# Optimization experiments

Hardware: AMD Instinct MI355X
Metric: run time of the kernel (lower is better)

Reference implementation:

```python
import jax, jax.numpy as jnp
import numpy as np

H = 16      # num_heads
D = 64      # head_dim
BQ = 64     # block_size_q
BKV = 64    # block_size_kv


def setup_inputs() -> dict:
    key = jax.random.key(0)
    ks = jax.random.split(key, 5)
    B, S, dim = 2, 2048, 1024
    x = jax.random.normal(ks[0], (B, S, dim), dtype=jnp.float32)
    Wq = jax.random.normal(ks[1], (dim, H * D), dtype=jnp.float32) * 0.02
    Wk = jax.random.normal(ks[2], (dim, H * D), dtype=jnp.float32) * 0.02
    Wv = jax.random.normal(ks[3], (dim, H * D), dtype=jnp.float32) * 0.02
    Wo = jax.random.normal(ks[4], (H * D, dim), dtype=jnp.float32) * 0.02
    return {"x": x, "Wq": Wq, "Wk": Wk, "Wv": Wv, "Wo": Wo}


def _flash_tiled(q, k, v, scale):
    # q,k,v: (B, H, S, D). Non-causal tiled attention with online softmax,
    # faithfully replicating the source's per-iteration division by l_new.
    B, nh, S, d = q.shape
    nq, nkv = S // BQ, S // BKV
    qb = q.reshape(B, nh, nq, BQ, d)                       # all q blocks at once (outer loop vectorized)
    kb = k.reshape(B, nh, nkv, BKV, d).transpose(2, 0, 1, 3, 4)  # (nkv, B, H, BKV, D)
    vb = v.reshape(B, nh, nkv, BKV, d).transpose(2, 0, 1, 3, 4)

    o0 = jnp.zeros((B, nh, nq, BQ, d), q.dtype)
    m0 = jnp.full((B, nh, nq, BQ), -jnp.inf, q.dtype)
    l0 = jnp.zeros((B, nh, nq, BQ), q.dtype)

    def step(carry, kv):
        o, m, l = carry
        kj, vj = kv
        s = jnp.einsum('bhnqd,bhkd->bhnqk', qb, kj) * scale   # (B,H,nq,BQ,BKV)
        m_new = jnp.maximum(m, s.max(axis=-1))
        p = jnp.exp(s - m_new[..., None])
        alpha = jnp.exp(m - m_new)
        l_new = alpha * l + p.sum(axis=-1)
        # NOTE: division by l_new every iteration, as in the source module.
        o_new = (alpha[..., None] * o + jnp.einsum('bhnqk,bhkd->bhnqd', p, vj)) / l_new[..., None]
        return (o_new, m_new, l_new), None

    (o, _, _), _ = jax.lax.scan(step, (o0, m0, l0), (kb, vb))
    return o.reshape(B, nh, S, d)


def reference(x, Wq, Wk, Wv, Wo):
    B, S, dim = x.shape
    scale = D ** -0.5
    q = (x @ Wq).reshape(B, S, H, D).transpose(0, 2, 1, 3)
    k = (x @ Wk).reshape(B, S, H, D).transpose(0, 2, 1, 3)
    v = (x @ Wv).reshape(B, S, H, D).transpose(0, 2, 1, 3)
    o = _flash_tiled(q, k, v, scale)                       # (B,H,S,D)
    out = o.transpose(0, 2, 1, 3).reshape(B, S, H * D)
    return out @ Wo
```

## Files before the change

kernel.cpp:

```cpp
#include <hip/hip_runtime.h>
#include <hip/hip_bf16.h>
#include <math.h>

#define BB   2
#define SS   2048
#define DIM  1024
#define NH   16
#define HD   64
#define MTOT (BB * SS)

typedef unsigned short ushortT;
typedef __attribute__((ext_vector_type(8))) short short8v;
typedef __attribute__((ext_vector_type(4))) float float4v;
typedef __attribute__((ext_vector_type(16))) float float16v;

union FragU { short8v v; unsigned short us[8]; unsigned int u[4]; };

__device__ inline unsigned short f2bf(float x) {
    unsigned u = __builtin_bit_cast(unsigned, x);
    u += 0x7fffu + ((u >> 16) & 1u);
    return (unsigned short)(u >> 16);
}
__device__ inline float bf2f(unsigned short h) {
    unsigned u = ((unsigned)h) << 16;
    return __builtin_bit_cast(float, u);
}
__device__ inline void split_tr(float x, unsigned short& hi, unsigned short& lo) {
    unsigned u = __builtin_bit_cast(unsigned, x);
    hi = (unsigned short)(u >> 16);
    float hf = __builtin_bit_cast(float, u & 0xffff0000u);
    lo = (unsigned short)(__builtin_bit_cast(unsigned, x - hf) >> 16);
}
__device__ inline void split4(const float4& x, short4& hi, short4& lo) {
    unsigned short h0 = f2bf(x.x), h1 = f2bf(x.y), h2 = f2bf(x.z), h3 = f2bf(x.w);
    hi = make_short4((short)h0, (short)h1, (short)h2, (short)h3);
    lo = make_short4((short)f2bf(x.x - bf2f(h0)), (short)f2bf(x.y - bf2f(h1)),
                     (short)f2bf(x.z - bf2f(h2)), (short)f2bf(x.w - bf2f(h3)));
}
__device__ inline void gld_lds16(const void* g, void* l) {
    __builtin_amdgcn_global_load_lds(
        (const __attribute__((address_space(1))) void*)g,
        (__attribute__((address_space(3))) void*)l, 16, 0, 0);
}
__device__ inline unsigned cvt_pk_bf16(float a, float b) {
    unsigned r;
    asm("v_cvt_pk_bf16_f32 %0, %1, %2" : "=v"(r) : "v"(a), "v"(b));
    return r;
}
__device__ inline void permlane32_swap(unsigned &a, unsigned &b) {
    asm("v_permlane32_swap_b32 %0, %1" : "+v"(a), "+v"(b));
}

__global__ __launch_bounds__(256) void convert_split_kernel(
    const float* __restrict__ in, ushortT* __restrict__ hi, ushortT* __restrict__ lo, int n4)
{
    int t = blockIdx.x * 256 + threadIdx.x;
    if (t < n4) {
        float4 x = ((const float4*)in)[t];
        short4 h, l; split4(x, h, l);
        ((short4*)hi)[t] = h;
        ((short4*)lo)[t] = l;
    }
}

__global__ __launch_bounds__(256) void transpose_split_kernel(
    const float* __restrict__ W0, const float* __restrict__ W1,
    const float* __restrict__ W2, const float* __restrict__ W3,
    ushortT* __restrict__ WtH, ushortT* __restrict__ WtL)
{
    const int z = blockIdx.z;
    const float* __restrict__ W = (z == 0) ? W0 : (z == 1) ? W1 : (z == 2) ? W2 : W3;
    ushortT* H = WtH + (size_t)z * 1024 * 1024;
    ushortT* L = WtL + (size_t)z * 1024 * 1024;

    __shared__ float T[64][65];
    const int k0 = blockIdx.y * 64, n0 = blockIdx.x * 64;
    const int tid = threadIdx.x;
    const int c4 = (tid & 15) * 4;

#pragma unroll
    for (int i = 0; i < 4; i++) {
        int r = (tid >> 4) + 16 * i;
        *(float4*)&T[r][c4] = *(const float4*)(W + (size_t)(k0 + r) * 1024 + n0 + c4);
    }
    __syncthreads();
#pragma unroll
    for (int i = 0; i < 4; i++) {
        int n = (tid >> 4) + 16 * i;
        float4 vv = make_float4(T[c4 + 0][n], T[c4 + 1][n], T[c4 + 2][n], T[c4 + 3][n]);
        short4 h, l; split4(vv, h, l);
        *(short4*)&H[(size_t)(n0 + n) * 1024 + k0 + c4] = h;
        *(short4*)&L[(size_t)(n0 + n) * 1024 + k0 + c4] = l;
    }
}

__global__ __launch_bounds__(256) void kv_convert_kernel(
    const float* __restrict__ kw,
    ushortT* __restrict__ KhG, ushortT* __restrict__ KlG)
{
    const int jb = blockIdx.x, bh = blockIdx.y;
    const int b = bh >> 4, h = bh & 15;

    __shared__ float T[64][68];
    const int tid = threadIdx.x;
    const size_t ibase = (size_t)b * SS * DIM + (size_t)h * HD + (size_t)(jb * 64) * DIM;
    const int c4 = (tid & 15) * 4;
#pragma unroll
    for (int i = 0; i < 4; i++) {
        int r = (tid >> 4) + 16 * i;
        *(float4*)&T[r][c4] = *(const float4*)(kw + ibase + (size_t)r * DIM + c4);
    }
    __syncthreads();

    ushortT* oh = KhG + (size_t)(bh * 32 + jb) * 4096;
    ushortT* ol = KlG + (size_t)(bh * 32 + jb) * 4096;

#pragma unroll
    for (int i = 0; i < 2; i++) {
        const int s = tid + i * 256;
        const int f = s >> 6;
        const int lane = s & 63;
        const int ds = f >> 1, kvt = f & 1;
        const int kv = kvt * 32 + (lane & 31);
        const int d0 = ds * 16 + (lane >> 5) * 8;
        ushortT hv[8], lv[8];
#pragma unroll
        for (int j = 0; j < 8; j++) split_tr(T[kv][d0 + j], hv[j], lv[j]);
        *(short4*)&oh[s * 8]     = *(short4*)&hv[0];
        *(short4*)&oh[s * 8 + 4] = *(short4*)&hv[4];
        *(short4*)&ol[s * 8]     = *(short4*)&lv[0];
        *(short4*)&ol[s * 8 + 4] = *(short4*)&lv[4];
    }
}

__global__ __launch_bounds__(256, 2) void gemm_bt_split_kernel(
    const ushortT* __restrict__ Ah, const ushortT* __restrict__ Al,
    const ushortT* __restrict__ BtH, const ushortT* __restrict__ BtL,
    float* __restrict__ Y0, float* __restrict__ Y1,
    ushortT* __restrict__ VhG, ushortT* __restrict__ VlG)
{
    const int z = blockIdx.z;
    const ushortT* __restrict__ Bh = BtH + (size_t)z * 1024 * 1024;
    const ushortT* __restrict__ Bl = BtL + (size_t)z * 1024 * 1024;

    const int K = 1024, N = 1024;
    const int wid  = blockIdx.x + (blockIdx.y << 3);
    const int work = ((wid & 7) << 5) + (wid >> 3);
    const int m0 = (work >> 3) * 128;
    const int n0 = (work & 7) * 128;

    __shared__ __align__(16) ushortT AhS[128 * 64];
    __shared__ __align__(16) ushortT AlS[128 * 64];
    __shared__ __align__(16) ushortT BhS[128 * 64];
    __shared__ __align__(16) ushortT BlS[128 * 64];

    const int tid  = threadIdx.x;
    const int wave = tid >> 6, lane = tid & 63;
    const int quad = lane >> 4, l15 = lane & 15;
    const int wm = wave >> 1, wn = wave & 1;
    const int rx = l15 & 7;

    float4v acc[4][4];
#pragma unroll
    for (int i = 0; i < 4; i++)
#pragma unroll
        for (int j = 0; j < 4; j++) acc[i][j] = (float4v){0.f, 0.f, 0.f, 0.f};

    for (int k0 = 0; k0 < K; k0 += 64) {
        __syncthreads();
#pragma unroll
        for (int i = 0; i < 4; i++) {
            const int s = tid + i * 256;
            const int r = s >> 3;
            const int kk = ((s & 7) ^ (r & 7)) * 8;
            gld_lds16(Ah + (size_t)(m0 + r) * K + k0 + kk, &AhS[s * 8]);
            gld_lds16(Al + (size_t)(m0 + r) * K + k0 + kk, &AlS[s * 8]);
            gld_lds16(Bh + (size_t)(n0 + r) * K + k0 + kk, &BhS[s * 8]);
            gld_lds16(Bl + (size_t)(n0 + r) * K + k0 + kk, &BlS[s * 8]);
        }
        __syncthreads();

#pragma unroll
        for (int ks = 0; ks < 2; ks++) {
            FragU ah[4], al[4], bh[4], bl[4];
#pragma unroll
            for (int t = 0; t < 4; t++) {
                const int ra = wm * 64 + t * 16 + l15;
                const int rb = wn * 64 + t * 16 + l15;
                const int boff = ((ks * 4 + quad) ^ rx) * 8;
                ah[t].v = *(const short8v*)&AhS[ra * 64 + boff];
                al[t].v = *(const short8v*)&AlS[ra * 64 + boff];
                bh[t].v = *(const short8v*)&BhS[rb * 64 + boff];
                bl[t].v = *(const short8v*)&BlS[rb * 64 + boff];
            }
#pragma unroll
            for (int mt = 0; mt < 4; mt++)
#pragma unroll
                for (int nt = 0; nt < 4; nt++) {
                    acc[mt][nt] = __builtin_amdgcn_mfma_f32_16x16x32_bf16(ah[mt].v, bh[nt].v, acc[mt][nt], 0, 0, 0);
                    acc[mt][nt] = __builtin_amdgcn_mfma_f32_16x16x32_bf16(ah[mt].v, bl[nt].v, acc[mt][nt], 0, 0, 0);
                    acc[mt][nt] = __builtin_amdgcn_mfma_f32_16x16x32_bf16(al[mt].v, bh[nt].v, acc[mt][nt], 0, 0, 0);
                }
        }
    }

    if (z == 2) {
        const int b  = m0 >> 11;
        const int jb = ((m0 & 2047) >> 6) + wm;
        const int h  = (n0 >> 6) + wn;
        const size_t tb = (size_t)((b * 16 + h) * 32 + jb) * 4096;
        ushortT* vh = VhG + tb;
        ushortT* vl = VlG + tb;
#pragma unroll
        for (int mt = 0; mt < 4; mt++)
#pragma unroll
            for (int nt = 0; nt < 4; nt++) {
                const int off = ((((nt >> 1) * 4 + mt) * 64 +
                                  (quad >> 1) * 32 + (nt & 1) * 16 + l15) * 8) +
                                (quad & 1) * 4;
                float4 vv = make_float4(acc[mt][nt][0], acc[mt][nt][1],
                                        acc[mt][nt][2], acc[mt][nt][3]);
                unsigned short h0, l0, h1, l1, h2, l2, h3, l3;
                split_tr(vv.x, h0, l0); split_tr(vv.y, h1, l1);
                split_tr(vv.z, h2, l2); split_tr(vv.w, h3, l3);
                *(short4*)&vh[off] = make_short4((short)h0, (short)h1, (short)h2, (short)h3);
                *(short4*)&vl[off] = make_short4((short)l0, (short)l1, (short)l2, (short)l3);
            }
    } else {
        float* __restrict__ Y = (z == 0) ? Y0 : Y1;
#pragma unroll
        for (int mt = 0; mt < 4; mt++)
#pragma unroll
            for (int r = 0; r < 4; r++) {
                const int row = m0 + wm * 64 + mt * 16 + quad * 4 + r;
                float* yp = Y + (size_t)row * N + n0 + wn * 64 + l15;
#pragma unroll
                for (int nt = 0; nt < 4; nt++)
                    yp[nt * 16] = acc[mt][nt][r];
            }
    }
}

__global__ __launch_bounds__(256, 2) void gemm_bt64_kernel(
    const ushortT* __restrict__ Ah, const ushortT* __restrict__ Al,
    const ushortT* __restrict__ Bh, const ushortT* __restrict__ Bl,
    float* __restrict__ Y)
{
    const int K = 1024, N = 1024;
    const int wid  = blockIdx.x + (blockIdx.y << 3);
    const int work = ((wid & 7) << 6) + (wid >> 3);
    const int m0 = (work >> 3) * 64;
    const int n0 = (work & 7) * 128;

    __shared__ __align__(16) ushortT AhS[64 * 64];
    __shared__ __align__(16) ushortT AlS[64 * 64];
    __shared__ __align__(16) ushortT BhS[128 * 64];
    __shared__ __align__(16) ushortT BlS[128 * 64];

    const int tid  = threadIdx.x;
    const int wave = tid >> 6, lane = tid & 63;
    const int quad = lane >> 4, l15 = lane & 15;
    const int rx = l15 & 7;

    float4v acc[4][2];
#pragma unroll
    for (int i = 0; i < 4; i++)
#pragma unroll
        for (int j = 0; j < 2; j++) acc[i][j] = (float4v){0.f, 0.f, 0.f, 0.f};

    for (int k0 = 0; k0 < K; k0 += 64) {
        __syncthreads();
#pragma unroll
        for (int i = 0; i < 2; i++) {
            const int s = tid + i * 256;
            const int r = s >> 3;
            const int kk = ((s & 7) ^ (r & 7)) * 8;
            gld_lds16(Ah + (size_t)(m0 + r) * K + k0 + kk, &AhS[s * 8]);
            gld_lds16(Al + (size_t)(m0 + r) * K + k0 + kk, &AlS[s * 8]);
        }
#pragma unroll
        for (int i = 0; i < 4; i++) {
            const int s = tid + i * 256;
            const int r = s >> 3;
            const int kk = ((s & 7) ^ (r & 7)) * 8;
            gld_lds16(Bh + (size_t)(n0 + r) * K + k0 + kk, &BhS[s * 8]);
            gld_lds16(Bl + (size_t)(n0 + r) * K + k0 + kk, &BlS[s * 8]);
        }
        __syncthreads();

#pragma unroll
        for (int ks = 0; ks < 2; ks++) {
            FragU ah[4], al[4], bh[2], bl[2];
#pragma unroll
            for (int t = 0; t < 4; t++) {
                const int ra = t * 16 + l15;
                const int boff = ((ks * 4 + quad) ^ rx) * 8;
                ah[t].v = *(const short8v*)&AhS[ra * 64 + boff];
                al[t].v = *(const short8v*)&AlS[ra * 64 + boff];
            }
#pragma unroll
            for (int t = 0; t < 2; t++) {
                const int rb = wave * 32 + t * 16 + l15;
                const int boff = ((ks * 4 + quad) ^ rx) * 8;
                bh[t].v = *(const short8v*)&BhS[rb * 64 + boff];
                bl[t].v = *(const short8v*)&BlS[rb * 64 + boff];
            }
#pragma unroll
            for (int mt = 0; mt < 4; mt++)
#pragma unroll
                for (int nt = 0; nt < 2; nt++) {
                    acc[mt][nt] = __builtin_amdgcn_mfma_f32_16x16x32_bf16(ah[mt].v, bh[nt].v, acc[mt][nt], 0, 0, 0);
                    acc[mt][nt] = __builtin_amdgcn_mfma_f32_16x16x32_bf16(ah[mt].v, bl[nt].v, acc[mt][nt], 0, 0, 0);
                    acc[mt][nt] = __builtin_amdgcn_mfma_f32_16x16x32_bf16(al[mt].v, bh[nt].v, acc[mt][nt], 0, 0, 0);
                }
        }
    }

#pragma unroll
    for (int mt = 0; mt < 4; mt++)
#pragma unroll
        for (int r = 0; r < 4; r++) {
            const int row = m0 + mt * 16 + quad * 4 + r;
            float* yp = Y + (size_t)row * N + n0 + wave * 32 + l15;
#pragma unroll
            for (int nt = 0; nt < 2; nt++)
                yp[nt * 16] = acc[mt][nt][r];
        }
}

__global__ __launch_bounds__(256, 2) void attn_mfma_kernel(
    const float* __restrict__ q,
    const ushortT* __restrict__ KhG, const ushortT* __restrict__ KlG,
    const ushortT* __restrict__ VhG, const ushortT* __restrict__ VlG,
    ushortT* __restrict__ Oh, ushortT* __restrict__ Ol)
{
    __shared__ __align__(16) ushortT SMEM[32768];

    const int tid  = threadIdx.x;
    const int wave = tid >> 6, lane = tid & 63;
    const int l31 = lane & 31, hi5 = lane >> 5;
    const int wid  = blockIdx.x + (blockIdx.y << 4);
    const int work = ((wid & 7) << 6) + (wid >> 3);
    const int qx = work & 15;
    const int bh = work >> 4;
    const int b = bh >> 4, h = bh & 15;
    const size_t base = (size_t)b * SS * DIM + (size_t)h * HD;
    const int qs0 = qx * 128 + wave * 32;
    const int lane8 = lane * 8;
    const int sl0 = wave * 128 + lane, sl1 = sl0 + 64;

    ushortT* K0 = SMEM;
    ushortT* K1 = SMEM + 8192;
    ushortT* V0 = SMEM + 16384;
    ushortT* V1 = SMEM + 24576;

    const float qscale = 0.125f * 1.4426950408889634f;
    FragU Qh[4], Ql[4];
    {
        const int qrow = qs0 + l31;
#pragma unroll
        for (int ds = 0; ds < 4; ds++) {
            const float* p0 = q + base + (size_t)qrow * DIM + ds * 16 + hi5 * 8;
            float4 a = *(const float4*)(p0);
            float4 c = *(const float4*)(p0 + 4);
            float e[8] = {a.x, a.y, a.z, a.w, c.x, c.y, c.z, c.w};
#pragma unroll
            for (int j = 0; j < 8; j++) {
                float x = e[j] * qscale;
                unsigned short hs = f2bf(x);
                Qh[ds].us[j] = hs;
                Ql[ds].us[j] = f2bf(x - bf2f(hs));
            }
        }
    }

    float16v Oacc[2];
#pragma unroll
    for (int dt = 0; dt < 2; dt++)
        Oacc[dt] = (float16v){0.f,0.f,0.f,0.f,0.f,0.f,0.f,0.f,
                              0.f,0.f,0.f,0.f,0.f,0.f,0.f,0.f};

    float m_run = -INFINITY;
    float l_run = 0.f;
    float inv_prev = 1.0f;

    auto stage_K = [&](int t, ushortT* dst) {
        const size_t tb = (size_t)(bh * 32 + t) * 4096;
        gld_lds16(KhG + tb + sl0 * 8, &dst[sl0 * 8]);
        gld_lds16(KhG + tb + sl1 * 8, &dst[sl1 * 8]);
        gld_lds16(KlG + tb + sl0 * 8, &dst[4096 + sl0 * 8]);
        gld_lds16(KlG + tb + sl1 * 8, &dst[4096 + sl1 * 8]);
    };
    auto stage_V = [&](int t, ushortT* dst) {
        const size_t tb = (size_t)(bh * 32 + t) * 4096;
        gld_lds16(VhG + tb + sl0 * 8, &dst[sl0 * 8]);
        gld_lds16(VhG + tb + sl1 * 8, &dst[sl1 * 8]);
        gld_lds16(VlG + tb + sl0 * 8, &dst[4096 + sl0 * 8]);
        gld_lds16(VlG + tb + sl1 * 8, &dst[4096 + sl1 * 8]);
    };

    auto qk = [&](const ushortT* Kb, float16v (&st)[2]) {
        const ushortT* KhS = Kb;
        const ushortT* KlS = Kb + 4096;
#pragma unroll
        for (int t = 0; t < 2; t++)
            st[t] = (float16v){0.f,0.f,0.f,0.f,0.f,0.f,0.f,0.f,
                               0.f,0.f,0.f,0.f,0.f,0.f,0.f,0.f};
#pragma unroll
        for (int ds = 0; ds < 4; ds++) {
            FragU kh0, kl0, kh1, kl1;
            kh0.v = *(const short8v*)&KhS[(ds * 2 + 0) * 512 + lane8];
            kl0.v = *(const short8v*)&KlS[(ds * 2 + 0) * 512 + lane8];
            kh1.v = *(const short8v*)&KhS[(ds * 2 + 1) * 512 + lane8];
            kl1.v = *(const short8v*)&KlS[(ds * 2 + 1) * 512 + lane8];
            st[0] = __builtin_amdgcn_mfma_f32_32x32x16_bf16(kh0.v, Qh[ds].v, st[0], 0, 0, 0);
            st[0] = __builtin_amdgcn_mfma_f32_32x32x16_bf16(kh0.v, Ql[ds].v, st[0], 0, 0, 0);
            st[0] = __builtin_amdgcn_mfma_f32_32x32x16_bf16(kl0.v, Qh[ds].v, st[0], 0, 0, 0);
            st[1] = __builtin_amdgcn_mfma_f32_32x32x16_bf16(kh1.v, Qh[ds].v, st[1], 0, 0, 0);
            st[1] = __builtin_amdgcn_mfma_f32_32x32x16_bf16(kh1.v, Ql[ds].v, st[1], 0, 0, 0);
            st[1] = __builtin_amdgcn_mfma_f32_32x32x16_bf16(kl1.v, Qh[ds].v, st[1], 0, 0, 0);
        }
    };

    auto finish = [&](float16v (&st)[2], const ushortT* Vb) {
        const ushortT* VhS = Vb;
        const ushortT* VlS = Vb + 4096;
        float wscale;
        {
            float g[8];
#pragma unroll
            for (int t = 0; t < 2; t++)
#pragma unroll
                for (int i = 0; i < 4; i++)
                    g[t * 4 + i] = fmaxf(fmaxf(st[t][4 * i], st[t][4 * i + 1]),
                                         fmaxf(st[t][4 * i + 2], st[t][4 * i + 3]));
            float vmax = fmaxf(fmaxf(fmaxf(g[0], g[1]), fmaxf(g[2], g[3])),
                               fmaxf(fmaxf(g[4], g[5]), fmaxf(g[6], g[7])));
            vmax = fmaxf(vmax, __shfl_xor(vmax, 32, 64));
            const float mn = fmaxf(m_run, vmax);
            const float al = __builtin_amdgcn_exp2f(m_run - mn);

            float ssum = 0.f;
#pragma unroll
            for (int t = 0; t < 2; t++)
#pragma unroll
                for (int r = 0; r < 16; r++) {
                    const float p = __builtin_amdgcn_exp2f(st[t][r] - mn);
                    st[t][r] = p;
                    ssum += p;
                }
            ssum += __shfl_xor(ssum, 32, 64);
            const float ln = al * l_run + ssum;
            wscale = al * inv_prev;
            inv_prev = __builtin_amdgcn_rcpf(ln);
            m_run = mn;
            l_run = ln;
        }

#pragma unroll
        for (int dt = 0; dt < 2; dt++)
#pragma unroll
            for (int r = 0; r < 16; r++)
                Oacc[dt][r] *= wscale;

#pragma unroll
        for (int kvs = 0; kvs < 4; kvs++) {
            const int kvt = kvs >> 1;
            const int R = (kvs & 1) * 8;
            float p0 = st[kvt][R + 0], p1 = st[kvt][R + 1];
            float p2 = st[kvt][R + 2], p3 = st[kvt][R + 3];
            float p4 = st[kvt][R + 4], p5 = st[kvt][R + 5];
            float p6 = st[kvt][R + 6], p7 = st[kvt][R + 7];
            unsigned X0 = cvt_pk_bf16(p0, p1), X1 = cvt_pk_bf16(p2, p3);
            unsigned Y0 = cvt_pk_bf16(p4, p5), Y1 = cvt_pk_bf16(p6, p7);
            float e0 = p0 - __builtin_bit_cast(float, X0 << 16);
            float e1 = p1 - __builtin_bit_cast(float, X0 & 0xffff0000u);
            float e2 = p2 - __builtin_bit_cast(float, X1 << 16);
            float e3 = p3 - __builtin_bit_cast(float, X1 & 0xffff0000u);
            float e4 = p4 - __builtin_bit_cast(float, Y0 << 16);
            float e5 = p5 - __builtin_bit_cast(float, Y0 & 0xffff0000u);
            float e6 = p6 - __builtin_bit_cast(float, Y1 << 16);
            float e7 = p7 - __builtin_bit_cast(float, Y1 & 0xffff0000u);
            unsigned Z0 = cvt_pk_bf16(e0, e1), Z1 = cvt_pk_bf16(e2, e3);
            unsigned W0 = cvt_pk_bf16(e4, e5), W1 = cvt_pk_bf16(e6, e7);
            permlane32_swap(X0, Y0);
            permlane32_swap(X1, Y1);
            permlane32_swap(Z0, W0);
            permlane32_swap(Z1, W1);
            FragU Phf, Plf;
            Phf.u[0] = X0; Phf.u[1] = X1; Phf.u[2] = Y0; Phf.u[3] = Y1;
            Plf.u[0] = Z0; Plf.u[1] = Z1; Plf.u[2] = W0; Plf.u[3] = W1;

#pragma unroll
            for (int dt = 0; dt < 2; dt++) {
                FragU vh, vl;
                vh.v = *(const short8v*)&VhS[(dt * 4 + kvs) * 512 + lane8];
                vl.v = *(const short8v*)&VlS[(dt * 4 + kvs) * 512 + lane8];
                Oacc[dt] = __builtin_amdgcn_mfma_f32_32x32x16_bf16(vh.v, Phf.v, Oacc[dt], 0, 0, 0);
                Oacc[dt] = __builtin_amdgcn_mfma_f32_32x32x16_bf16(vl.v, Phf.v, Oacc[dt], 0, 0, 0);
                Oacc[dt] = __builtin_amdgcn_mfma_f32_32x32x16_bf16(vh.v, Plf.v, Oacc[dt], 0, 0, 0);
            }
        }
    };

    float16v stA[2], stB[2];

    stage_K(0, K0);
    stage_K(1, K1);
    stage_V(0, V0);
    __syncthreads();
    qk(K0, stA);
    __syncthreads();

    auto iter = [&](int jb, float16v (&SC)[2], float16v (&SN)[2],
                    ushortT* Kc, ushortT* Kn, ushortT* Vc, ushortT* Vn) {
        if (jb <= 29) stage_K(jb + 2, Kc);
        if (jb <= 30) stage_V(jb + 1, Vn);
        if (jb <= 30) qk(Kn, SN);
        finish(SC, Vc);
        __syncthreads();
    };

    for (int jb = 0; jb < 32; jb += 2) {
        iter(jb,     stA, stB, K0, K1, V0, V1);
        iter(jb + 1, stB, stA, K1, K0, V1, V0);
    }

#pragma unroll
    for (int dt = 0; dt < 2; dt++)
#pragma unroll
        for (int r = 0; r < 16; r++)
            Oacc[dt][r] *= inv_prev;

    float* EP = ((float*)SMEM) + wave * 1056;
    const int qq = lane >> 1, dh = (lane & 1) * 16;
#pragma unroll
    for (int dt = 0; dt < 2; dt++) {
#pragma unroll
        for (int g = 0; g < 4; g++) {
            float4 wv = make_float4(Oacc[dt][4 * g + 0], Oacc[dt][4 * g + 1],
                                    Oacc[dt][4 * g + 2], Oacc[dt][4 * g + 3]);
            *(float4*)&EP[l31 * 33 + g * 8 + hi5 * 4] = wv;
        }
        float vals[16];
#pragma unroll
        for (int k4 = 0; k4 < 4; k4++)
            *(float4*)&vals[k4 * 4] = *(const float4*)&EP[qq * 33 + dh + k4 * 4];

        unsigned ho[8], lo8[8];
#pragma unroll
        for (int kk = 0; kk < 8; kk++) {
            unsigned short h0, l0, h1, l1;
            split_tr(vals[2 * kk], h0, l0);
            split_tr(vals[2 * kk + 1], h1, l1);
            ho[kk]  = (unsigned)h0 | ((unsigned)h1 << 16);
            lo8[kk] = (unsigned)l0 | ((unsigned)l1 << 16);
        }
        const int qrow = qs0 + qq;
        const size_t off = (size_t)(b * SS + qrow) * DIM + h * HD + dt * 32 + dh;
        *(uint4*)&Oh[off]     = make_uint4(ho[0], ho[1], ho[2], ho[3]);
        *(uint4*)&Oh[off + 8] = make_uint4(ho[4], ho[5], ho[6], ho[7]);
        *(uint4*)&Ol[off]     = make_uint4(lo8[0], lo8[1], lo8[2], lo8[3]);
        *(uint4*)&Ol[off + 8] = make_uint4(lo8[4], lo8[5], lo8[6], lo8[7]);
    }
}

extern "C" void kernel_launch(void* const* d_in, const int* in_sizes, int n_in,
                              void* d_out, int out_size, void* d_ws, size_t ws_size,
                              hipStream_t stream)
{
    const float* x  = (const float*)d_in[0];
    const float* Wq = (const float*)d_in[1];
    const float* Wk = (const float*)d_in[2];
    const float* Wv = (const float*)d_in[3];
    const float* Wo = (const float*)d_in[4];
    float* out = (float*)d_out;

    char* w = (char*)d_ws;
    float*   qw  = (float*)(w);
    float*   kw  = (float*)(w + ((size_t)16 << 20));
    ushortT* VhG = (ushortT*)(w + ((size_t)32 << 20));
    ushortT* VlG = (ushortT*)(w + ((size_t)40 << 20));
    ushortT* XhS = (ushortT*)(w + ((size_t)48 << 20));
    ushortT* XlS = (ushortT*)(w + ((size_t)56 << 20));
    ushortT* WtH = (ushortT*)(w + ((size_t)64 << 20));
    ushortT* WtL = (ushortT*)(w + ((size_t)72 << 20));
    ushortT* KhG = (ushortT*)(w + ((size_t)80 << 20));
    ushortT* KlG = (ushortT*)(w + ((size_t)88 << 20));
    ushortT* OhS = (ushortT*)kw;
    ushortT* OlS = (ushortT*)(w + ((size_t)24 << 20));

    dim3 blk(256);
    const int n4 = MTOT * DIM / 4;

    convert_split_kernel<<<dim3(n4 / 256), blk, 0, stream>>>(x, XhS, XlS, n4);
    transpose_split_kernel<<<dim3(16, 16, 4), blk, 0, stream>>>(Wq, Wk, Wv, Wo, WtH, WtL);

    gemm_bt_split_kernel<<<dim3(8, 32, 3), blk, 0, stream>>>(
        XhS, XlS, WtH, WtL, qw, kw, VhG, VlG);

    kv_convert_kernel<<<dim3(32, 32), blk, 0, stream>>>(kw, KhG, KlG);

    attn_mfma_kernel<<<dim3(16, 32), blk, 0, stream>>>(qw, KhG, KlG, VhG, VlG, OhS, OlS);

    gemm_bt64_kernel<<<dim3(8, 64), blk, 0, stream>>>(
        OhS, OlS, WtH + (size_t)3 * 1024 * 1024, WtL + (size_t)3 * 1024 * 1024,
        out);
}
```

Baseline: 284.3 us.

## Double-buffer LDS in split-bf16 GEMM kernels with 32-wide K stages

Both projection GEMM kernels now use two LDS buffers with a K-step of 32 instead of one buffer with a K-step of 64. The next stage's global-to-LDS loads are issued before computing on the current buffer, removing the load-then-barrier-then-compute serialization. The XOR swizzle is adapted to 4-chunk rows. Halving the K-step doubles the number of barriers, and the asynchronous LDS loads rely on the barrier to make data visible, so overlap depends on how the compiler places vmcnt waits.

Result: slower. 306.3 us (+7.7%).

```diff
diff --git a/kernel.cpp b/kernel.cpp
--- a/kernel.cpp
+++ b/kernel.cpp
@@ -149,16 +149,13 @@
     const int m0 = (work >> 3) * 128;
     const int n0 = (work & 7) * 128;
 
-    __shared__ __align__(16) ushortT AhS[128 * 64];
-    __shared__ __align__(16) ushortT AlS[128 * 64];
-    __shared__ __align__(16) ushortT BhS[128 * 64];
-    __shared__ __align__(16) ushortT BlS[128 * 64];
+    __shared__ __align__(16) ushortT SMEM[32768];
 
     const int tid  = threadIdx.x;
     const int wave = tid >> 6, lane = tid & 63;
     const int quad = lane >> 4, l15 = lane & 15;
     const int wm = wave >> 1, wn = wave & 1;
-    const int rx = l15 & 7;
+    const int rk = (l15 ^ (l15 >> 2)) & 3;
 
     float4v acc[4][4];
 #pragma unroll
@@ -166,42 +163,54 @@
 #pragma unroll
         for (int j = 0; j < 4; j++) acc[i][j] = (float4v){0.f, 0.f, 0.f, 0.f};
 
-    for (int k0 = 0; k0 < K; k0 += 64) {
+    auto stage = [&](int t, int bsel) {
+        ushortT* S = SMEM + bsel * 16384;
+        const int k0 = t * 32;
+#pragma unroll
+        for (int i = 0; i < 2; i++) {
+            const int s = tid + i * 256;
+            const int r = s >> 2;
+            const int kk = (((s & 3) ^ (r ^ (r >> 2))) & 3) * 8;
+            gld_lds16(Ah + (size_t)(m0 + r) * K + k0 + kk, &S[s * 8]);
+            gld_lds16(Al + (size_t)(m0 + r) * K + k0 + kk, &S[4096 + s * 8]);
+            gld_lds16(Bh + (size_t)(n0 + r) * K + k0 + kk, &S[8192 + s * 8]);
+            gld_lds16(Bl + (size_t)(n0 + r) * K + k0 + kk, &S[12288 + s * 8]);
+        }
+    };
+
+    auto compute = [&](int bsel) {
+        const ushortT* S = SMEM + bsel * 16384;
+        FragU ah[4], al[4], bh[4], bl[4];
+        const int boff = (quad ^ rk) * 8;
+#pragma unroll
+        for (int t = 0; t < 4; t++) {
+            const int ra = wm * 64 + t * 16 + l15;
+            const int rb = wn * 64 + t * 16 + l15;
+            ah[t].v = *(const short8v*)&S[ra * 32 + boff];
+            al[t].v = *(const short8v*)&S[4096 + ra * 32 + boff];
+            bh[t].v = *(const short8v*)&S[8192 + rb * 32 + boff];
+            bl[t].v = *(const short8v*)&S[12288 + rb * 32 + boff];
+        }
+#pragma unroll
+        for (int mt = 0; mt < 4; mt++)
+#pragma unroll
+            for (int nt = 0; nt < 4; nt++) {
+                acc[mt][nt] = __builtin_amdgcn_mfma_f32_16x16x32_bf16(ah[mt].v, bh[nt].v, acc[mt][nt], 0, 0, 0);
+                acc[mt][nt] = __builtin_amdgcn_mfma_f32_16x16x32_bf16(ah[mt].v, bl[nt].v, acc[mt][nt], 0, 0, 0);
+                acc[mt][nt] = __builtin_amdgcn_mfma_f32_16x16x32_bf16(al[mt].v, bh[nt].v, acc[mt][nt], 0, 0, 0);
+            }
+    };
+
+    stage(0, 0);
+    __syncthreads();
+
+    for (int t = 0; t < 32; t += 2) {
+        if (t < 31) stage(t + 1, 1);
+        compute(0);
         __syncthreads();
-#pragma unroll
-        for (int i = 0; i < 4; i++) {
-            const int s = tid + i * 256;
-            const int r = s >> 3;
-            const int kk = ((s & 7) ^ (r & 7)) * 8;
-            gld_lds16(Ah + (size_t)(m0 + r) * K + k0 + kk, &AhS[s * 8]);
-            gld_lds16(Al + (size_t)(m0 + r) * K + k0 + kk, &AlS[s * 8]);
-            gld_lds16(Bh + (size_t)(n0 + r) * K + k0 + kk, &BhS[s * 8]);
-            gld_lds16(Bl + (size_t)(n0 + r) * K + k0 + kk, &BlS[s * 8]);
-        }
+        if (t + 2 < 32) stage(t + 2, 0);
+        compute(1);
         __syncthreads();
-
-#pragma unroll
-        for (int ks = 0; ks < 2; ks++) {
-            FragU ah[4], al[4], bh[4], bl[4];
-#pragma unroll
-            for (int t = 0; t < 4; t++) {
-                const int ra = wm * 64 + t * 16 + l15;
-                const int rb = wn * 64 + t * 16 + l15;
-                const int boff = ((ks * 4 + quad) ^ rx) * 8;
-                ah[t].v = *(const short8v*)&AhS[ra * 64 + boff];
-                al[t].v = *(const short8v*)&AlS[ra * 64 + boff];
-                bh[t].v = *(const short8v*)&BhS[rb * 64 + boff];
-                bl[t].v = *(const short8v*)&BlS[rb * 64 + boff];
-            }
-#pragma unroll
-            for (int mt = 0; mt < 4; mt++)
-#pragma unroll
-                for (int nt = 0; nt < 4; nt++) {
-                    acc[mt][nt] = __builtin_amdgcn_mfma_f32_16x16x32_bf16(ah[mt].v, bh[nt].v, acc[mt][nt], 0, 0, 0);
-                    acc[mt][nt] = __builtin_amdgcn_mfma_f32_16x16x32_bf16(ah[mt].v, bl[nt].v, acc[mt][nt], 0, 0, 0);
-                    acc[mt][nt] = __builtin_amdgcn_mfma_f32_16x16x32_bf16(al[mt].v, bh[nt].v, acc[mt][nt], 0, 0, 0);
-                }
-        }
     }
 
     if (z == 2) {
@@ -252,15 +261,12 @@
     const int m0 = (work >> 3) * 64;
     const int n0 = (work & 7) * 128;
 
-    __shared__ __align__(16) ushortT AhS[64 * 64];
-    __shared__ __align__(16) ushortT AlS[64 * 64];
-    __shared__ __align__(16) ushortT BhS[128 * 64];
-    __shared__ __align__(16) ushortT BlS[128 * 64];
+    __shared__ __align__(16) ushortT SMEM[24576];
 
     const int tid  = threadIdx.x;
     const int wave = tid >> 6, lane = tid & 63;
     const int quad = lane >> 4, l15 = lane & 15;
-    const int rx = l15 & 7;
+    const int rk = (l15 ^ (l15 >> 2)) & 3;
 
     float4v acc[4][2];
 #pragma unroll
@@ -268,52 +274,62 @@
 #pragma unroll
         for (int j = 0; j < 2; j++) acc[i][j] = (float4v){0.f, 0.f, 0.f, 0.f};
 
-    for (int k0 = 0; k0 < K; k0 += 64) {
-        __syncthreads();
+    auto stage = [&](int t, int bsel) {
+        ushortT* S = SMEM + bsel * 12288;
+        const int k0 = t * 32;
+        {
+            const int s = tid;
+            const int r = s >> 2;
+            const int kk = (((s & 3) ^ (r ^ (r >> 2))) & 3) * 8;
+            gld_lds16(Ah + (size_t)(m0 + r) * K + k0 + kk, &S[s * 8]);
+            gld_lds16(Al + (size_t)(m0 + r) * K + k0 + kk, &S[2048 + s * 8]);
+        }
 #pragma unroll
         for (int i = 0; i < 2; i++) {
             const int s = tid + i * 256;
-            const int r = s >> 3;
-            const int kk = ((s & 7) ^ (r & 7)) * 8;
-            gld_lds16(Ah + (size_t)(m0 + r) * K + k0 + kk, &AhS[s * 8]);
-            gld_lds16(Al + (size_t)(m0 + r) * K + k0 + kk, &AlS[s * 8]);
-        }
-#pragma unroll
-        for (int i = 0; i < 4; i++) {
-            const int s = tid + i * 256;
-            const int r = s >> 3;
-            const int kk = ((s & 7) ^ (r & 7)) * 8;
-            gld_lds16(Bh + (size_t)(n0 + r) * K + k0 + kk, &BhS[s * 8]);
-            gld_lds16(Bl + (size_t)(n0 + r) * K + k0 + kk, &BlS[s * 8]);
-        }
+            const int r = s >> 2;
+            const int kk = (((s & 3) ^ (r ^ (r >> 2))) & 3) * 8;
+            gld_lds16(Bh + (size_t)(n0 + r) * K + k0 + kk, &S[4096 + s * 8]);
+            gld_lds16(Bl + (size_t)(n0 + r) * K + k0 + kk, &S[8192 + s * 8]);
+        }
+    };
+
+    auto compute = [&](int bsel) {
+        const ushortT* S = SMEM + bsel * 12288;
+        FragU ah[4], al[4], bh[2], bl[2];
+        const int boff = (quad ^ rk) * 8;
+#pragma unroll
+        for (int t = 0; t < 4; t++) {
+            const int ra = t * 16 + l15;
+            ah[t].v = *(const short8v*)&S[ra * 32 + boff];
+            al[t].v = *(const short8v*)&S[2048 + ra * 32 + boff];
+        }
+#pragma unroll
+        for (int t = 0; t < 2; t++) {
+            const int rb = wave * 32 + t * 16 + l15;
+            bh[t].v = *(const short8v*)&S[4096 + rb * 32 + boff];
+            bl[t].v = *(const short8v*)&S[8192 + rb * 32 + boff];
+        }
+#pragma unroll
+        for (int mt = 0; mt < 4; mt++)
+#pragma unroll
+            for (int nt = 0; nt < 2; nt++) {
+                acc[mt][nt] = __builtin_amdgcn_mfma_f32_16x16x32_bf16(ah[mt].v, bh[nt].v, acc[mt][nt], 0, 0, 0);
+                acc[mt][nt] = __builtin_amdgcn_mfma_f32_16x16x32_bf16(ah[mt].v, bl[nt].v, acc[mt][nt], 0, 0, 0);
+                acc[mt][nt] = __builtin_amdgcn_mfma_f32_16x16x32_bf16(al[mt].v, bh[nt].v, acc[mt][nt], 0, 0, 0);
+            }
+    };
+
+    stage(0, 0);
+    __syncthreads();
+
+    for (int t = 0; t < 32; t += 2) {
+        if (t < 31) stage(t + 1, 1);
+        compute(0);
         __syncthreads();
-
-#pragma unroll
-        for (int ks = 0; ks < 2; ks++) {
-            FragU ah[4], al[4], bh[2], bl[2];
-#pragma unroll
-            for (int t = 0; t < 4; t++) {
-                const int ra = t * 16 + l15;
-                const int boff = ((ks * 4 + quad) ^ rx) * 8;
-                ah[t].v = *(const short8v*)&AhS[ra * 64 + boff];
-                al[t].v = *(const short8v*)&AlS[ra * 64 + boff];
-            }
-#pragma unroll
-            for (int t = 0; t < 2; t++) {
-                const int rb = wave * 32 + t * 16 + l15;
-                const int boff = ((ks * 4 + quad) ^ rx) * 8;
-                bh[t].v = *(const short8v*)&BhS[rb * 64 + boff];
-                bl[t].v = *(const short8v*)&BlS[rb * 64 + boff];
-            }
-#pragma unroll
-            for (int mt = 0; mt < 4; mt++)
-#pragma unroll
-                for (int nt = 0; nt < 2; nt++) {
-                    acc[mt][nt] = __builtin_amdgcn_mfma_f32_16x16x32_bf16(ah[mt].v, bh[nt].v, acc[mt][nt], 0, 0, 0);
-                    acc[mt][nt] = __builtin_amdgcn_mfma_f32_16x16x32_bf16(ah[mt].v, bl[nt].v, acc[mt][nt], 0, 0, 0);
-                    acc[mt][nt] = __builtin_amdgcn_mfma_f32_16x16x32_bf16(al[mt].v, bh[nt].v, acc[mt][nt], 0, 0, 0);
-                }
-        }
+        if (t + 2 < 32) stage(t + 2, 0);
+        compute(1);
+        __syncthreads();
     }
 
 #pragma unroll
```
